# Optimization experiments

Hardware: AMD Instinct MI355X
Metric: run time of the kernel (lower is better)

Reference implementation:

```python
import jax, jax.numpy as jnp
import numpy as np
from jax import lax


def _layernorm(x, g, b, eps=1e-5):
    mu = x.mean(-1, keepdims=True)
    var = ((x - mu) ** 2).mean(-1, keepdims=True)
    return (x - mu) * lax.rsqrt(var + eps) * g + b


def _conv1d(x, w, b):
    # x: (B, T, Cin), w: (K, Cin, Cout) -> (B, T, Cout), SAME padding
    return lax.conv_general_dilated(x, w, (1,), 'SAME',
                                    dimension_numbers=('NWC', 'WIO', 'NWC')) + b


def _gated(x, wf, bf, wg, bg):
    return jax.nn.relu(_conv1d(x, wf, bf)) * jax.nn.sigmoid(_conv1d(x, wg, bg))


def setup_inputs() -> dict:
    key = jax.random.key(0)
    ks = iter(jax.random.split(key, 32))
    B, T, F, H = 32, 1024, 64, 768
    ch = H // 3
    d = {'x': jax.random.normal(next(ks), (B, T, F), jnp.float32)}
    for k in (3, 5, 7):
        d[f'conv{k}_wf'] = jax.random.normal(next(ks), (k, F, ch), jnp.float32) * 0.05
        d[f'conv{k}_bf'] = jnp.zeros((ch,), jnp.float32)
        d[f'conv{k}_wg'] = jax.random.normal(next(ks), (k, F, ch), jnp.float32) * 0.05
        d[f'conv{k}_bg'] = jnp.zeros((ch,), jnp.float32)
    d['conv_ln_g'] = jnp.ones((H,), jnp.float32)
    d['conv_ln_b'] = jnp.zeros((H,), jnp.float32)
    for name in ('gqa_wq', 'gqa_wk', 'gqa_wv', 'gqa_wp'):
        d[name] = jax.random.normal(next(ks), (2, H, H), jnp.float32) * 0.02
    d['gqa_bp'] = jnp.zeros((2, H), jnp.float32)
    d['gqa_ln_g'] = jnp.ones((2, H), jnp.float32)
    d['gqa_ln_b'] = jnp.zeros((2, H), jnp.float32)
    d['proj_w'] = jax.random.normal(next(ks), (2 * H, H), jnp.float32) * 0.02
    d['proj_b'] = jnp.zeros((H,), jnp.float32)
    d['proj_ln_g'] = jnp.ones((H,), jnp.float32)
    d['proj_ln_b'] = jnp.zeros((H,), jnp.float32)
    return d


def _gqa(h, wq, wk, wv, wp, bp, ln_g, ln_b, n_groups=4):
    B, T, H = h.shape
    G, D = n_groups, H // n_groups
    scale = D ** -0.5
    Q = (h @ wq).reshape(B, T, G, D)
    K = (h @ wk).reshape(B, T, G, D)
    V = (h @ wv).reshape(B, T, G, D)
    attn = jax.nn.softmax(jnp.einsum('bqgd,bkgd->bgqk', Q, K) * scale, axis=-1)
    out = jnp.einsum('bgqk,bkgd->bqgd', attn, V).reshape(B, T, H)
    return _layernorm(h + out @ wp + bp, ln_g, ln_b)


def reference(x, conv3_wf, conv3_bf, conv3_wg, conv3_bg,
              conv5_wf, conv5_bf, conv5_wg, conv5_bg,
              conv7_wf, conv7_bf, conv7_wg, conv7_bg,
              conv_ln_g, conv_ln_b,
              gqa_wq, gqa_wk, gqa_wv, gqa_wp, gqa_bp, gqa_ln_g, gqa_ln_b,
              proj_w, proj_b, proj_ln_g, proj_ln_b):
    # Multi-scale gated conv front end (SAME padding -> all branches length T)
    o3 = _gated(x, conv3_wf, conv3_bf, conv3_wg, conv3_bg)
    o5 = _gated(x, conv5_wf, conv5_bf, conv5_wg, conv5_bg)
    o7 = _gated(x, conv7_wf, conv7_bf, conv7_wg, conv7_bg)
    h = _layernorm(jnp.concatenate([o3, o5, o7], axis=-1), conv_ln_g, conv_ln_b)
    # Two GQA blocks
    for i in range(2):
        h = _gqa(h, gqa_wq[i], gqa_wk[i], gqa_wv[i], gqa_wp[i],
                 gqa_bp[i], gqa_ln_g[i], gqa_ln_b[i])
    # mean + population-std pooling over time
    m = h.mean(axis=1)
    s = jnp.sqrt(((h - m[:, None, :]) ** 2).mean(axis=1))
    z = jnp.concatenate([m, s], axis=-1) @ proj_w + proj_b
    return jax.nn.relu(_layernorm(z, proj_ln_g, proj_ln_b))
```

## Files before the change

kernel.cpp:

```cpp
#include <hip/hip_runtime.h>
#include <hip/hip_bf16.h>


constexpr int Bb = 32, Tt = 1024, Ff = 64, Hh = 768, Gg = 4, Dd = 192;
constexpr float EPS = 1e-5f;
constexpr int WKMAX = 448;

typedef __attribute__((ext_vector_type(8))) short short8;
typedef __attribute__((ext_vector_type(4))) float floatx4;

__device__ __forceinline__ void async_copy16(const void* g, void* l) {
  __builtin_amdgcn_global_load_lds(
      (const __attribute__((address_space(1))) unsigned int*)g,
      (__attribute__((address_space(3))) unsigned int*)l, 16, 0, 0);
}

__device__ __forceinline__ short bf16s(float f) {
  __hip_bfloat16 h = __float2bfloat16(f);
  return *(short*)&h;
}

__device__ __forceinline__ unsigned int pack_bf16(float lo, float hi) {
  return (unsigned int)(unsigned short)bf16s(lo) |
         ((unsigned int)(unsigned short)bf16s(hi) << 16);
}

__device__ __forceinline__ float2 block_reduce2(float a, float b, float* tmp) {
  int lane = threadIdx.x & 63, wid = threadIdx.x >> 6;
#pragma unroll
  for (int off = 32; off > 0; off >>= 1) {
    a += __shfl_down(a, off);
    b += __shfl_down(b, off);
  }
  if (lane == 0) { tmp[wid] = a; tmp[4 + wid] = b; }
  __syncthreads();
  if (threadIdx.x == 0) {
    tmp[0] = tmp[0] + tmp[1] + tmp[2] + tmp[3];
    tmp[4] = tmp[4] + tmp[5] + tmp[6] + tmp[7];
  }
  __syncthreads();
  float2 r; r.x = tmp[0]; r.y = tmp[4];
  return r;
}

__global__ __launch_bounds__(256) void wt_cast_kernel(
    const float* __restrict__ wq, const float* __restrict__ wk,
    const float* __restrict__ wv, const float* __restrict__ wp,
    __hip_bfloat16* __restrict__ wt) {
  const int z = blockIdx.z;
  const int m = z & 3, i = z >> 2;
  const float* src =
      (m == 0 ? wq : m == 1 ? wk : m == 2 ? wv : wp) + (size_t)i * Hh * Hh;
  const float sc = (m == 0) ? 0.0721687836f : 1.f;
  __shared__ float tile[32][33];
  const int n0 = blockIdx.x * 32, k0 = blockIdx.y * 32;
  const int tx = threadIdx.x & 31, ty = threadIdx.x >> 5;
#pragma unroll
  for (int r = 0; r < 4; r++)
    tile[ty + 8 * r][tx] = src[(size_t)(k0 + ty + 8 * r) * Hh + n0 + tx];
  __syncthreads();
#pragma unroll
  for (int r = 0; r < 4; r++)
    wt[((size_t)z * Hh + n0 + ty + 8 * r) * Hh + k0 + tx] =
        __float2bfloat16(tile[tx][ty + 8 * r] * sc);
}

__global__ __launch_bounds__(256) void wcv_cast_kernel(
    const float* __restrict__ wf3, const float* __restrict__ wg3,
    const float* __restrict__ wf5, const float* __restrict__ wg5,
    const float* __restrict__ wf7, const float* __restrict__ wg7,
    __hip_bfloat16* __restrict__ wcv) {
  int idx = blockIdx.x * 256 + threadIdx.x;
  if (idx >= 3 * 512 * WKMAX) return;
  int j = idx / (512 * WKMAX);
  int rem = idx - j * 512 * WKMAX;
  int n = rem / WKMAX, k = rem % WKMAX;
  int Kw = 3 + 2 * j;
  float v = 0.f;
  if (k < Kw * 64) {
    const float* src = (n < 256) ? (j == 0 ? wf3 : j == 1 ? wf5 : wf7)
                                 : (j == 0 ? wg3 : j == 1 ? wg5 : wg7);
    v = src[(size_t)k * 256 + (n & 255)];
  }
  wcv[idx] = __float2bfloat16(v);
}

__global__ __launch_bounds__(256) void x_cast_kernel(
    const float* __restrict__ x, short* __restrict__ x16, int n8) {
  int idx = blockIdx.x * 256 + threadIdx.x;
  if (idx >= n8) return;
  const float4 a = ((const float4*)x)[idx * 2];
  const float4 b = ((const float4*)x)[idx * 2 + 1];
  short8 o;
  o[0] = bf16s(a.x); o[1] = bf16s(a.y); o[2] = bf16s(a.z); o[3] = bf16s(a.w);
  o[4] = bf16s(b.x); o[5] = bf16s(b.y); o[6] = bf16s(b.z); o[7] = bf16s(b.w);
  ((short8*)x16)[idx] = o;
}

__global__ __launch_bounds__(256) void conv_gemm_kernel(
    const short* __restrict__ x16, const short* __restrict__ wcv,
    short* __restrict__ yraw, int b0) {
  __shared__ __align__(16) short Asl[128 * 72];
  __shared__ __align__(16) short Bsl[128 * 72];
  const int t0 = blockIdx.x * 128, n0 = blockIdx.y * 128;
  const int bl = blockIdx.z / 3, j = blockIdx.z % 3;
  const int Kw = 3 + 2 * j, pad = j + 1;
  const int bglob = b0 + bl;
  const short* wb = wcv + (size_t)j * 512 * WKMAX;
  const int tid = threadIdx.x;
  const int lane = tid & 63;
  const int w = tid >> 6, wm = w >> 1, wn = w & 1;
  const int lm = lane & 15, quad = lane >> 4;

  floatx4 acc[4][4];
#pragma unroll
  for (int i = 0; i < 4; i++)
#pragma unroll
    for (int jj = 0; jj < 4; jj++) acc[i][jj] = (floatx4)0.f;

  for (int kk = 0; kk < Kw; kk++) {
    __syncthreads();
#pragma unroll
    for (int it = 0; it < 4; it++) {
      int s = it * 256 + tid;
      int row = s >> 3, c8 = s & 7;
      int t = t0 + row + kk - pad;
      short8 av = (short8)0;
      if (t >= 0 && t < Tt)
        av = *(const short8*)&x16[((size_t)bglob * Tt + t) * Ff + c8 * 8];
      *(short8*)&Asl[row * 72 + c8 * 8] = av;
      short8 bv = *(const short8*)&wb[(size_t)(n0 + row) * WKMAX + kk * 64 +
                                      c8 * 8];
      *(short8*)&Bsl[row * 72 + c8 * 8] = bv;
    }
    __syncthreads();
#pragma unroll
    for (int ks = 0; ks < 2; ks++) {
      short8 a[4], b[4];
#pragma unroll
      for (int i = 0; i < 4; i++)
        a[i] = *(const short8*)&Asl[(wm * 64 + i * 16 + lm) * 72 + ks * 32 +
                                    quad * 8];
#pragma unroll
      for (int jj = 0; jj < 4; jj++)
        b[jj] = *(const short8*)&Bsl[(wn * 64 + jj * 16 + lm) * 72 + ks * 32 +
                                     quad * 8];
#pragma unroll
      for (int i = 0; i < 4; i++)
#pragma unroll
        for (int jj = 0; jj < 4; jj++)
          acc[i][jj] = __builtin_amdgcn_mfma_f32_16x16x32_bf16(a[i], b[jj],
                                                               acc[i][jj],
                                                               0, 0, 0);
    }
  }

  const int rbase = quad * 4;
#pragma unroll
  for (int i = 0; i < 4; i++)
#pragma unroll
    for (int jj = 0; jj < 4; jj++) {
      int mrow = t0 + wm * 64 + i * 16 + rbase;
      int ncol = n0 + wn * 64 + jj * 16 + lm;
#pragma unroll
      for (int r = 0; r < 4; r++)
        yraw[((size_t)bl * Tt + mrow + r) * 1536 + j * 512 + ncol] =
            bf16s(acc[i][jj][r]);
    }
}

__global__ __launch_bounds__(256) void gate_ln_kernel(
    const short* __restrict__ yraw, __hip_bfloat16* __restrict__ h16,
    const float* __restrict__ bf3, const float* __restrict__ bg3,
    const float* __restrict__ bf5, const float* __restrict__ bg5,
    const float* __restrict__ bf7, const float* __restrict__ bg7,
    const float* __restrict__ g, const float* __restrict__ bt) {
  __shared__ float red[8];
  const size_t row = blockIdx.x;
  float v[3], s = 0.f, ss = 0.f;
#pragma unroll
  for (int jj = 0; jj < 3; jj++) {
    int c = threadIdx.x + jj * 256;
    int br = c >> 8, cc = c & 255;
    const float* bfp = br == 0 ? bf3 : br == 1 ? bf5 : bf7;
    const float* bgp = br == 0 ? bg3 : br == 1 ? bg5 : bg7;
    __hip_bfloat16 rf = *(const __hip_bfloat16*)&yraw[row * 1536 + br * 512 + cc];
    __hip_bfloat16 rg =
        *(const __hip_bfloat16*)&yraw[row * 1536 + br * 512 + 256 + cc];
    float f = __bfloat162float(rf) + bfp[cc];
    float gt = __bfloat162float(rg) + bgp[cc];
    float a = f > 0.f ? f : 0.f;
    float t = a * (1.f / (1.f + __expf(-gt)));
    v[jj] = t; s += t; ss += t * t;
  }
  float2 r = block_reduce2(s, ss, red);
  float mu = r.x * (1.f / Hh);
  float var = r.y * (1.f / Hh) - mu * mu;
  float rs = rsqrtf(var + EPS);
#pragma unroll
  for (int jj = 0; jj < 3; jj++) {
    int c = threadIdx.x + jj * 256;
    float o = (v[jj] - mu) * rs * g[c] + bt[c];
    h16[row * Hh + c] = __float2bfloat16(o);
  }
}

__global__ __launch_bounds__(256) void res_ln_kernel(
    __hip_bfloat16* __restrict__ h16, const __hip_bfloat16* __restrict__ y,
    const float* __restrict__ bp, const float* __restrict__ g,
    const float* __restrict__ bt) {
  __shared__ float red[8];
  const size_t row = blockIdx.x;
  float v[3], s = 0.f, ss = 0.f;
#pragma unroll
  for (int jj = 0; jj < 3; jj++) {
    int c = threadIdx.x + jj * 256;
    float t = __bfloat162float(h16[row * Hh + c]) +
              __bfloat162float(y[row * Hh + c]) + bp[c];
    v[jj] = t; s += t; ss += t * t;
  }
  float2 r = block_reduce2(s, ss, red);
  float mu = r.x * (1.f / Hh);
  float var = r.y * (1.f / Hh) - mu * mu;
  float rs = rsqrtf(var + EPS);
#pragma unroll
  for (int jj = 0; jj < 3; jj++) {
    int c = threadIdx.x + jj * 256;
    float o = (v[jj] - mu) * rs * g[c] + bt[c];
    h16[row * Hh + c] = __float2bfloat16(o);
  }
}

__global__ __launch_bounds__(256) void gemm_qkv(
    const short* __restrict__ A, const short* __restrict__ Bt,
    short* __restrict__ q16, short* __restrict__ k16,
    short* __restrict__ vt16) {
  constexpr int K = 768;
  __shared__ __align__(16) short Asl[128 * 32];
  __shared__ __align__(16) short Bsl[128 * 32];
  const int n0 = blockIdx.x * 128, m0 = blockIdx.y * 128;
  const int lane = threadIdx.x & 63;
  const int w = threadIdx.x >> 6, wm = w >> 1, wn = w & 1;
  const int lm = lane & 15, quad = lane >> 4;

  floatx4 acc[4][4];
#pragma unroll
  for (int i = 0; i < 4; i++)
#pragma unroll
    for (int jj = 0; jj < 4; jj++) acc[i][jj] = (floatx4)0.f;

  for (int k0 = 0; k0 < K; k0 += 32) {
    __syncthreads();
#pragma unroll
    for (int half = 0; half < 2; half++) {
      int s = half * 256 + threadIdx.x;
      int m = s >> 2, ks = (s & 3) * 8;
      async_copy16(&A[(size_t)(m0 + m) * K + k0 + ks], &Asl[s * 8]);
      async_copy16(&Bt[(size_t)(n0 + m) * K + k0 + ks], &Bsl[s * 8]);
    }
    __syncthreads();

    short8 a[4], b[4];
#pragma unroll
    for (int i = 0; i < 4; i++)
      a[i] = *(const short8*)&Asl[(wm * 64 + i * 16 + lm) * 32 + quad * 8];
#pragma unroll
    for (int jj = 0; jj < 4; jj++)
      b[jj] = *(const short8*)&Bsl[(wn * 64 + jj * 16 + lm) * 32 + quad * 8];
#pragma unroll
    for (int i = 0; i < 4; i++)
#pragma unroll
      for (int jj = 0; jj < 4; jj++)
        acc[i][jj] = __builtin_amdgcn_mfma_f32_16x16x32_bf16(a[i], b[jj],
                                                             acc[i][jj],
                                                             0, 0, 0);
  }

  const int which = blockIdx.x / 6;
  const int rbase = quad * 4;
#pragma unroll
  for (int i = 0; i < 4; i++)
#pragma unroll
    for (int jj = 0; jj < 4; jj++) {
      int mrow = m0 + wm * 64 + i * 16 + rbase;
      int nl = n0 - which * Hh + wn * 64 + jj * 16 + lm;
      if (which == 0) {
#pragma unroll
        for (int r = 0; r < 4; r++)
          q16[(size_t)(mrow + r) * Hh + nl] = bf16s(acc[i][jj][r]);
      } else if (which == 1) {
#pragma unroll
        for (int r = 0; r < 4; r++)
          k16[(size_t)(mrow + r) * Hh + nl] = bf16s(acc[i][jj][r]);
      } else {
        int bL = mrow >> 10, t = mrow & 1023;
        int g = nl / Dd, d = nl % Dd;
        short4 sv;
        sv.x = bf16s(acc[i][jj][0]); sv.y = bf16s(acc[i][jj][1]);
        sv.z = bf16s(acc[i][jj][2]); sv.w = bf16s(acc[i][jj][3]);
        *(short4*)&vt16[(((size_t)bL * Gg + g) * Dd + d) * Tt + t] = sv;
      }
    }
}

__global__ __launch_bounds__(256) void gemm_proj(
    const short* __restrict__ A, const short* __restrict__ Bt,
    short* __restrict__ C) {
  constexpr int K = 768, N = 768;
  __shared__ __align__(16) short Asl[128 * 32];
  __shared__ __align__(16) short Bsl[128 * 32];
  const int n0 = blockIdx.x * 128, m0 = blockIdx.y * 128;
  const int lane = threadIdx.x & 63;
  const int w = threadIdx.x >> 6, wm = w >> 1, wn = w & 1;
  const int lm = lane & 15, quad = lane >> 4;

  floatx4 acc[4][4];
#pragma unroll
  for (int i = 0; i < 4; i++)
#pragma unroll
    for (int jj = 0; jj < 4; jj++) acc[i][jj] = (floatx4)0.f;

  for (int k0 = 0; k0 < K; k0 += 32) {
    __syncthreads();
#pragma unroll
    for (int half = 0; half < 2; half++) {
      int s = half * 256 + threadIdx.x;
      int m = s >> 2, ks = (s & 3) * 8;
      async_copy16(&A[(size_t)(m0 + m) * K + k0 + ks], &Asl[s * 8]);
      async_copy16(&Bt[(size_t)(n0 + m) * K + k0 + ks], &Bsl[s * 8]);
    }
    __syncthreads();

    short8 a[4], b[4];
#pragma unroll
    for (int i = 0; i < 4; i++)
      a[i] = *(const short8*)&Asl[(wm * 64 + i * 16 + lm) * 32 + quad * 8];
#pragma unroll
    for (int jj = 0; jj < 4; jj++)
      b[jj] = *(const short8*)&Bsl[(wn * 64 + jj * 16 + lm) * 32 + quad * 8];
#pragma unroll
    for (int i = 0; i < 4; i++)
#pragma unroll
      for (int jj = 0; jj < 4; jj++)
        acc[i][jj] = __builtin_amdgcn_mfma_f32_16x16x32_bf16(a[i], b[jj],
                                                             acc[i][jj],
                                                             0, 0, 0);
  }

  const int rbase = quad * 4;
#pragma unroll
  for (int i = 0; i < 4; i++)
#pragma unroll
    for (int jj = 0; jj < 4; jj++) {
      int mrow = m0 + wm * 64 + i * 16 + rbase;
      int ncol = n0 + wn * 64 + jj * 16 + lm;
#pragma unroll
      for (int r = 0; r < 4; r++)
        C[(size_t)(mrow + r) * N + ncol] = bf16s(acc[i][jj][r]);
    }
}

__global__ __launch_bounds__(256, 2) void attn_mfma(
    const short* __restrict__ q16, const short* __restrict__ k16,
    const short* __restrict__ vt16, short* __restrict__ o16, int chunk4) {
  const int bg = blockIdx.x % chunk4;
  const int qb = blockIdx.x / chunk4;
  const int b = bg >> 2, g = bg & 3;
  const int q0 = qb * 128;
  const int tid = threadIdx.x;
  const int w = tid >> 6, lane = tid & 63, lm = lane & 15, quad = lane >> 4;

  __shared__ __align__(16) short Ks[2][32 * 200];
  __shared__ __align__(16) short Vt[2][208 * 32];
  constexpr int VBUF = 208 * 32;

  for (int e = tid; e < 2 * 16 * 32; e += 256) {
    int buf = e >> 9;
    int r = e & 511;
    Vt[buf][192 * 32 + r] = (r < 32) ? (short)0x3F80 : (short)0;
  }

  short8 qf[2][6];
#pragma unroll
  for (int mt = 0; mt < 2; mt++)
#pragma unroll
    for (int ks = 0; ks < 6; ks++) {
      int tok = b * Tt + q0 + w * 32 + mt * 16 + lm;
      qf[mt][ks] = *(const short8*)&q16[(size_t)tok * Hh + g * Dd + ks * 32 +
                                        quad * 8];
    }

  floatx4 Oa[2][13];
#pragma unroll
  for (int mt = 0; mt < 2; mt++)
#pragma unroll
    for (int n = 0; n < 13; n++) Oa[mt][n] = (floatx4)0.f;

  int krow[3], kcs[3];
  const short* kgp[3];
  const short* vgp[3];
  short* vld[3];
#pragma unroll
  for (int it = 0; it < 3; it++) {
    int s = it * 256 + tid;
    krow[it] = s / 24; kcs[it] = s - krow[it] * 24;
    kgp[it] = &k16[(size_t)(b * Tt + krow[it]) * Hh + g * Dd + kcs[it] * 8];
    vgp[it] = &vt16[(((size_t)b * Gg + g) * Dd + (s >> 2)) * Tt + (s & 3) * 8];
    vld[it] = (short*)&Vt[0][0] + (size_t)s * 8;
  }

  short8 kvK[3];
#pragma unroll
  for (int it = 0; it < 3; it++) kvK[it] = *(const short8*)kgp[it];
#pragma unroll
  for (int it = 0; it < 3; it++)
    *(short8*)&Ks[0][krow[it] * 200 + kcs[it] * 8] = kvK[it];
#pragma unroll
  for (int it = 0; it < 3; it++)
    kvK[it] = *(const short8*)(kgp[it] + (size_t)32 * Hh);
#pragma unroll
  for (int it = 0; it < 3; it++) async_copy16(vgp[it], vld[it]);

  for (int i = 0; i < 32; i++) {
    const int ib = i & 1;
    __syncthreads();

    if (i + 1 < 32) {
#pragma unroll
      for (int it = 0; it < 3; it++)
        *(short8*)&Ks[ib ^ 1][krow[it] * 200 + kcs[it] * 8] = kvK[it];
      const int vo = (i + 1) * 32;
#pragma unroll
      for (int it = 0; it < 3; it++)
        async_copy16(vgp[it] + vo, vld[it] + (ib ^ 1) * VBUF);
      if (i + 2 < 32) {
        const size_t ko = (size_t)(i + 2) * 32 * Hh;
#pragma unroll
        for (int it = 0; it < 3; it++)
          kvK[it] = *(const short8*)(kgp[it] + ko);
      }
    }

    floatx4 st[2][2];
#pragma unroll
    for (int mt = 0; mt < 2; mt++)
#pragma unroll
      for (int jj = 0; jj < 2; jj++) st[mt][jj] = (floatx4)0.f;
#pragma unroll
    for (int ks = 0; ks < 6; ks++) {
      short8 k0 = *(const short8*)&Ks[ib][lm * 200 + ks * 32 + quad * 8];
      short8 k1 = *(const short8*)&Ks[ib][(16 + lm) * 200 + ks * 32 + quad * 8];
      st[0][0] = __builtin_amdgcn_mfma_f32_16x16x32_bf16(k0, qf[0][ks], st[0][0], 0, 0, 0);
      st[0][1] = __builtin_amdgcn_mfma_f32_16x16x32_bf16(k1, qf[0][ks], st[0][1], 0, 0, 0);
      st[1][0] = __builtin_amdgcn_mfma_f32_16x16x32_bf16(k0, qf[1][ks], st[1][0], 0, 0, 0);
      st[1][1] = __builtin_amdgcn_mfma_f32_16x16x32_bf16(k1, qf[1][ks], st[1][1], 0, 0, 0);
    }

    short8 ptf[2];
#pragma unroll
    for (int mt = 0; mt < 2; mt++) {
      float p[2][4];
#pragma unroll
      for (int jj = 0; jj < 2; jj++)
#pragma unroll
        for (int r = 0; r < 4; r++) p[jj][r] = __expf(st[mt][jj][r]);

      int pk00 = (int)pack_bf16(p[0][0], p[0][1]);
      int pk01 = (int)pack_bf16(p[0][2], p[0][3]);
      int pk10 = (int)pack_bf16(p[1][0], p[1][1]);
      int pk11 = (int)pack_bf16(p[1][2], p[1][3]);
      int srcA = ((quad & 1) << 5) + lm;
      int srcB = srcA + 16;
      int a0 = __shfl(pk00, srcA), a1 = __shfl(pk01, srcA);
      int a2 = __shfl(pk00, srcB), a3 = __shfl(pk01, srcB);
      int b0 = __shfl(pk10, srcA), b1 = __shfl(pk11, srcA);
      int b2 = __shfl(pk10, srcB), b3 = __shfl(pk11, srcB);
      bool hi = quad >= 2;
      union { int u[4]; short8 v; } pu;
      pu.u[0] = hi ? b0 : a0;
      pu.u[1] = hi ? b1 : a1;
      pu.u[2] = hi ? b2 : a2;
      pu.u[3] = hi ? b3 : a3;
      ptf[mt] = pu.v;
    }

#pragma unroll
    for (int n = 0; n < 13; n++) {
      short8 vf = *(const short8*)&Vt[ib][(n * 16 + lm) * 32 + quad * 8];
      Oa[0][n] = __builtin_amdgcn_mfma_f32_16x16x32_bf16(vf, ptf[0], Oa[0][n], 0, 0, 0);
      Oa[1][n] = __builtin_amdgcn_mfma_f32_16x16x32_bf16(vf, ptf[1], Oa[1][n], 0, 0, 0);
    }
  }

#pragma unroll
  for (int mt = 0; mt < 2; mt++) {
    float lval = __shfl(Oa[mt][12][0], lm);
    float inv = 1.f / lval;
    int tok = b * Tt + q0 + w * 32 + mt * 16 + lm;
#pragma unroll
    for (int n = 0; n < 12; n++) {
      short4 sv;
      sv.x = bf16s(Oa[mt][n][0] * inv);
      sv.y = bf16s(Oa[mt][n][1] * inv);
      sv.z = bf16s(Oa[mt][n][2] * inv);
      sv.w = bf16s(Oa[mt][n][3] * inv);
      *(short4*)&o16[(size_t)tok * Hh + g * Dd + n * 16 + quad * 4] = sv;
    }
  }
}

__global__ __launch_bounds__(256) void pool_stage1(
    const __hip_bfloat16* __restrict__ h16, float* __restrict__ ppart,
    int b0) {
  int idx = blockIdx.x * 256 + threadIdx.x;
  int seg = blockIdx.y;
  int bl = idx / Hh, c = idx % Hh;
  float s = 0.f, ss = 0.f;
  const __hip_bfloat16* hp = &h16[((size_t)bl * Tt + seg * 128) * Hh + c];
  for (int t = 0; t < 128; t++) {
    float v = __bfloat162float(hp[(size_t)t * Hh]);
    s += v; ss += v * v;
  }
  float* o = &ppart[(((size_t)(b0 + bl) * 8 + seg) * 2) * Hh + c];
  o[0] = s;
  o[Hh] = ss;
}

__global__ __launch_bounds__(256) void pool_stage2(
    const float* __restrict__ ppart, float* __restrict__ pool) {
  int idx = blockIdx.x * 256 + threadIdx.x;
  int b = idx / Hh, c = idx % Hh;
  float s = 0.f, ss = 0.f;
#pragma unroll
  for (int seg = 0; seg < 8; seg++) {
    const float* o = &ppart[(((size_t)b * 8 + seg) * 2) * Hh + c];
    s += o[0]; ss += o[Hh];
  }
  float mu = s * (1.f / Tt);
  float var = ss * (1.f / Tt) - mu * mu;
  pool[(size_t)b * 1536 + c] = mu;
  pool[(size_t)b * 1536 + 768 + c] = sqrtf(fmaxf(var, 0.f));
}

__global__ __launch_bounds__(256) void final_partial(
    const float* __restrict__ pool, const float* __restrict__ pw,
    float* __restrict__ part) {
  const int n = blockIdx.x * 256 + threadIdx.x;
  const int bg = blockIdx.y * 4;
  const int ks = blockIdx.z, k0 = ks * 192;
  __shared__ float ms[4][192];
  for (int e = threadIdx.x; e < 4 * 192; e += 256) {
    int bb = e / 192, kk = e % 192;
    ms[bb][kk] = pool[(size_t)(bg + bb) * 1536 + k0 + kk];
  }
  __syncthreads();
  float a0 = 0.f, a1 = 0.f, a2 = 0.f, a3 = 0.f;
  for (int kk = 0; kk < 192; kk++) {
    float wv = pw[(size_t)(k0 + kk) * Hh + n];
    a0 = fmaf(ms[0][kk], wv, a0);
    a1 = fmaf(ms[1][kk], wv, a1);
    a2 = fmaf(ms[2][kk], wv, a2);
    a3 = fmaf(ms[3][kk], wv, a3);
  }
  part[((size_t)ks * Bb + bg + 0) * Hh + n] = a0;
  part[((size_t)ks * Bb + bg + 1) * Hh + n] = a1;
  part[((size_t)ks * Bb + bg + 2) * Hh + n] = a2;
  part[((size_t)ks * Bb + bg + 3) * Hh + n] = a3;
}

__global__ __launch_bounds__(256) void final_stage2(
    const float* __restrict__ part, const float* __restrict__ pb,
    const float* __restrict__ g, const float* __restrict__ bt,
    float* __restrict__ out) {
  __shared__ float red[8];
  const int b = blockIdx.x;
  float v[3], s = 0.f, ss = 0.f;
#pragma unroll
  for (int jj = 0; jj < 3; jj++) {
    int n = threadIdx.x + jj * 256;
    float a = pb[n];
#pragma unroll
    for (int ks = 0; ks < 8; ks++) a += part[((size_t)ks * Bb + b) * Hh + n];
    v[jj] = a; s += a; ss += a * a;
  }
  float2 r = block_reduce2(s, ss, red);
  float mu = r.x * (1.f / Hh);
  float var = r.y * (1.f / Hh) - mu * mu;
  float rs = rsqrtf(var + EPS);
#pragma unroll
  for (int jj = 0; jj < 3; jj++) {
    int n = threadIdx.x + jj * 256;
    float o = (v[jj] - mu) * rs * g[n] + bt[n];
    out[(size_t)b * Hh + n] = o > 0.f ? o : 0.f;
  }
}

extern "C" void kernel_launch(void* const* d_in, const int* in_sizes, int n_in,
                              void* d_out, int out_size, void* d_ws,
                              size_t ws_size, hipStream_t stream) {
  (void)in_sizes; (void)n_in; (void)out_size;
  const float* x = (const float*)d_in[0];
  const float* cw[3][4];
  for (int j = 0; j < 3; j++)
    for (int p2 = 0; p2 < 4; p2++) cw[j][p2] = (const float*)d_in[1 + j * 4 + p2];
  const float* conv_ln_g = (const float*)d_in[13];
  const float* conv_ln_b = (const float*)d_in[14];
  const float* wq = (const float*)d_in[15];
  const float* wk = (const float*)d_in[16];
  const float* wv = (const float*)d_in[17];
  const float* wp = (const float*)d_in[18];
  const float* bp = (const float*)d_in[19];
  const float* lng = (const float*)d_in[20];
  const float* lnb = (const float*)d_in[21];
  const float* proj_w = (const float*)d_in[22];
  const float* proj_b = (const float*)d_in[23];
  const float* proj_ln_g = (const float*)d_in[24];
  const float* proj_ln_b = (const float*)d_in[25];
  float* out = (float*)d_out;

  const size_t perb = (size_t)Tt * Hh;
  const size_t fixedB = 8ull * Hh * Hh * 2 + 3ull * 512 * WKMAX * 2 +
                        (size_t)Bb * Tt * Ff * 2 + (size_t)Bb * 2 * Hh * 4 +
                        (size_t)Bb * 8 * 2 * Hh * 4 + 8ull * Bb * Hh * 4;
  int chunk = Bb;
  while (chunk > 1 && 8ull * perb * chunk + fixedB > ws_size) chunk >>= 1;

  const size_t crow = perb * (size_t)chunk;
  char* p = (char*)d_ws;
  __hip_bfloat16* h16 = (__hip_bfloat16*)p;  p += crow * 2;
  short* q16 = (short*)p;            p += crow * 2;
  short* k16 = (short*)p;            p += crow * 2;
  short* v16t = (short*)p;           p += crow * 2;
  short* yraw16 = q16;
  short* y16 = k16;
  __hip_bfloat16* wt = (__hip_bfloat16*)p;   p += 8ull * Hh * Hh * 2;
  __hip_bfloat16* wcv = (__hip_bfloat16*)p;  p += 3ull * 512 * WKMAX * 2;
  short* x16 = (short*)p;            p += (size_t)Bb * Tt * Ff * 2;
  float* pool = (float*)p;           p += (size_t)Bb * 2 * Hh * 4;
  float* ppart = (float*)p;          p += (size_t)Bb * 8 * 2 * Hh * 4;
  float* fpart = (float*)p;

  wt_cast_kernel<<<dim3(24, 24, 8), 256, 0, stream>>>(wq, wk, wv, wp, wt);
  wcv_cast_kernel<<<(3 * 512 * WKMAX + 255) / 256, 256, 0, stream>>>(
      cw[0][0], cw[0][2], cw[1][0], cw[1][2], cw[2][0], cw[2][2], wcv);
  x_cast_kernel<<<(Bb * Tt * Ff / 8 + 255) / 256, 256, 0, stream>>>(
      x, x16, Bb * Tt * Ff / 8);

  const short* wts = (const short*)wt;

  for (int b0 = 0; b0 < Bb; b0 += chunk) {
    const int M = chunk * Tt;

    conv_gemm_kernel<<<dim3(Tt / 128, 4, chunk * 3), 256, 0, stream>>>(
        x16, (const short*)wcv, yraw16, b0);
    gate_ln_kernel<<<M, 256, 0, stream>>>(
        yraw16, h16, cw[0][1], cw[0][3], cw[1][1], cw[1][3], cw[2][1],
        cw[2][3], conv_ln_g, conv_ln_b);

    for (int i = 0; i < 2; i++) {
      const short* wqkv = wts + (size_t)(i * 4) * Hh * Hh;
      const short* wtp = wts + (size_t)(i * 4 + 3) * Hh * Hh;
      gemm_qkv<<<dim3(18, M / 128), 256, 0, stream>>>((const short*)h16, wqkv,
                                                      q16, k16, v16t);
      attn_mfma<<<dim3(chunk * Gg * (Tt / 128)), 256, 0, stream>>>(
          q16, k16, v16t, q16, chunk * Gg);
      gemm_proj<<<dim3(6, M / 128), 256, 0, stream>>>(q16, wtp, y16);
      res_ln_kernel<<<M, 256, 0, stream>>>(h16, (const __hip_bfloat16*)y16,
                                           bp + (size_t)i * Hh,
                                           lng + (size_t)i * Hh,
                                           lnb + (size_t)i * Hh);
    }

    pool_stage1<<<dim3((chunk * Hh) / 256, 8), 256, 0, stream>>>(h16, ppart,
                                                                 b0);
  }

  pool_stage2<<<(Bb * Hh) / 256, 256, 0, stream>>>(ppart, pool);
  final_partial<<<dim3(3, 8, 8), 256, 0, stream>>>(pool, proj_w, fpart);
  final_stage2<<<Bb, 256, 0, stream>>>(fpart, proj_b, proj_ln_g, proj_ln_b,
                                       out);
}
```

Measured before the change: 990.6 us.

## Replace QKV and proj GEMMs with 256x256 tile, 4-stage async pipelined kernel

Merges the QKV and output-projection GEMMs into one templated kernel. It uses 256x256 tiles with 8 waves and a 4-deep ring of LDS buffers filled by async global-to-LDS copies, synchronised with explicit vmcnt waits and barriers. It also adds an XCD-aware block-index swizzle, a swizzled LDS layout to avoid bank conflicts, and raised wave priority around the MFMA block. The aim is to hide global load latency and raise MFMA utilisation, at the cost of 128KB of LDS and high register pressure that may limit occupancy.

```diff
diff --git a/kernel.cpp b/kernel.cpp
--- a/kernel.cpp
+++ b/kernel.cpp
@@ -231,133 +231,144 @@
   }
 }
 
-__global__ __launch_bounds__(256) void gemm_qkv(
+template <int MODE>
+__global__ __launch_bounds__(512, 2) void gemm_8ph(
     const short* __restrict__ A, const short* __restrict__ Bt,
-    short* __restrict__ q16, short* __restrict__ k16,
-    short* __restrict__ vt16) {
+    short* __restrict__ out_q, short* __restrict__ out_k,
+    short* __restrict__ out_v) {
   constexpr int K = 768;
-  __shared__ __align__(16) short Asl[128 * 32];
-  __shared__ __align__(16) short Bsl[128 * 32];
-  const int n0 = blockIdx.x * 128, m0 = blockIdx.y * 128;
-  const int lane = threadIdx.x & 63;
-  const int w = threadIdx.x >> 6, wm = w >> 1, wn = w & 1;
+  constexpr int NT = K / 32;
+  constexpr int NB = (MODE == 0) ? 9 : 3;
+  __shared__ __align__(16) short lds[4][16384];
+
+  const int nwg = gridDim.x;
+  const int qq = nwg >> 3, rr = nwg & 7;
+  const int xcd = blockIdx.x & 7, bidx = blockIdx.x >> 3;
+  const int swz =
+      (xcd < rr ? xcd * (qq + 1) : rr * (qq + 1) + (xcd - rr) * qq) + bidx;
+  const int nb = swz % NB, mb = swz / NB;
+  const int n0 = nb * 256, m0 = mb * 256;
+
+  const int tid = threadIdx.x;
+  const int lane = tid & 63, w = tid >> 6;
   const int lm = lane & 15, quad = lane >> 4;
-
-  floatx4 acc[4][4];
-#pragma unroll
-  for (int i = 0; i < 4; i++)
-#pragma unroll
-    for (int jj = 0; jj < 4; jj++) acc[i][jj] = (floatx4)0.f;
-
-  for (int k0 = 0; k0 < K; k0 += 32) {
-    __syncthreads();
-#pragma unroll
-    for (int half = 0; half < 2; half++) {
-      int s = half * 256 + threadIdx.x;
-      int m = s >> 2, ks = (s & 3) * 8;
-      async_copy16(&A[(size_t)(m0 + m) * K + k0 + ks], &Asl[s * 8]);
-      async_copy16(&Bt[(size_t)(n0 + m) * K + k0 + ks], &Bsl[s * 8]);
-    }
-    __syncthreads();
-
-    short8 a[4], b[4];
-#pragma unroll
-    for (int i = 0; i < 4; i++)
-      a[i] = *(const short8*)&Asl[(wm * 64 + i * 16 + lm) * 32 + quad * 8];
-#pragma unroll
-    for (int jj = 0; jj < 4; jj++)
-      b[jj] = *(const short8*)&Bsl[(wn * 64 + jj * 16 + lm) * 32 + quad * 8];
-#pragma unroll
-    for (int i = 0; i < 4; i++)
-#pragma unroll
-      for (int jj = 0; jj < 4; jj++)
-        acc[i][jj] = __builtin_amdgcn_mfma_f32_16x16x32_bf16(a[i], b[jj],
-                                                             acc[i][jj],
-                                                             0, 0, 0);
-  }
-
-  const int which = blockIdx.x / 6;
+  const int wm = w >> 2, wn = w & 3;
+
+  const short* sA[2];
+  const short* sB[2];
+  int dst[2];
+#pragma unroll
+  for (int li = 0; li < 2; li++) {
+    int l = li * 512 + tid;
+    int reg = l >> 6, cs = l & 63;
+    int cs2 = cs ^ (((cs >> 5) & 1) << 1);
+    int row = (reg << 4) + (cs2 >> 2);
+    int col = (cs2 & 3) << 3;
+    sA[li] = A + (size_t)(m0 + row) * K + col;
+    sB[li] = Bt + (size_t)(n0 + row) * K + col;
+    dst[li] = l * 8;
+  }
+
+#define STAGE8(kt, ring)                                   \
+  {                                                        \
+    const int _o = (kt) * 32;                              \
+    async_copy16(sA[0] + _o, &lds[ring][dst[0]]);          \
+    async_copy16(sB[0] + _o, &lds[ring][8192 + dst[0]]);   \
+    async_copy16(sA[1] + _o, &lds[ring][dst[1]]);          \
+    async_copy16(sB[1] + _o, &lds[ring][8192 + dst[1]]);   \
+  }
+
+  const int lane_sh = (lm * 32 + quad * 8) ^ ((lm >> 3) << 4);
+
+  floatx4 acc[8][4];
+#pragma unroll
+  for (int i = 0; i < 8; i++)
+#pragma unroll
+    for (int j = 0; j < 4; j++) acc[i][j] = (floatx4)0.f;
+
+  STAGE8(0, 0);
+  STAGE8(1, 1);
+  STAGE8(2, 2);
+  asm volatile("s_waitcnt vmcnt(8)" ::: "memory");
+  asm volatile("s_barrier" ::: "memory");
+  __builtin_amdgcn_sched_barrier(0);
+
+  for (int t = 0; t < NT; t++) {
+    const int ring = t & 3;
+    if (t + 3 < NT) STAGE8(t + 3, (t + 3) & 3);
+
+    short8 a[8], b[4];
+#pragma unroll
+    for (int i = 0; i < 8; i++)
+      a[i] = *(const short8*)&lds[ring][(wm * 8 + i) * 512 + lane_sh];
+#pragma unroll
+    for (int j = 0; j < 4; j++)
+      b[j] = *(const short8*)&lds[ring][8192 + (wn * 4 + j) * 512 + lane_sh];
+
+    __builtin_amdgcn_s_setprio(1);
+#pragma unroll
+    for (int i = 0; i < 8; i++)
+#pragma unroll
+      for (int j = 0; j < 4; j++)
+        acc[i][j] = __builtin_amdgcn_mfma_f32_16x16x32_bf16(a[i], b[j],
+                                                            acc[i][j],
+                                                            0, 0, 0);
+    __builtin_amdgcn_s_setprio(0);
+
+    if (t < NT - 1) {
+      if (t < NT - 3)
+        asm volatile("s_waitcnt vmcnt(8)" ::: "memory");
+      else if (t == NT - 3)
+        asm volatile("s_waitcnt vmcnt(4)" ::: "memory");
+      else
+        asm volatile("s_waitcnt vmcnt(0)" ::: "memory");
+      asm volatile("s_barrier" ::: "memory");
+      __builtin_amdgcn_sched_barrier(0);
+    }
+  }
+#undef STAGE8
+
   const int rbase = quad * 4;
-#pragma unroll
-  for (int i = 0; i < 4; i++)
-#pragma unroll
-    for (int jj = 0; jj < 4; jj++) {
-      int mrow = m0 + wm * 64 + i * 16 + rbase;
-      int nl = n0 - which * Hh + wn * 64 + jj * 16 + lm;
-      if (which == 0) {
+  if (MODE == 1) {
+#pragma unroll
+    for (int i = 0; i < 8; i++) {
+      const int mrow = m0 + wm * 128 + i * 16 + rbase;
+#pragma unroll
+      for (int j = 0; j < 4; j++) {
+        const int ncol = n0 + wn * 64 + j * 16 + lm;
 #pragma unroll
         for (int r = 0; r < 4; r++)
-          q16[(size_t)(mrow + r) * Hh + nl] = bf16s(acc[i][jj][r]);
-      } else if (which == 1) {
-#pragma unroll
-        for (int r = 0; r < 4; r++)
-          k16[(size_t)(mrow + r) * Hh + nl] = bf16s(acc[i][jj][r]);
-      } else {
-        int bL = mrow >> 10, t = mrow & 1023;
-        int g = nl / Dd, d = nl % Dd;
-        short4 sv;
-        sv.x = bf16s(acc[i][jj][0]); sv.y = bf16s(acc[i][jj][1]);
-        sv.z = bf16s(acc[i][jj][2]); sv.w = bf16s(acc[i][jj][3]);
-        *(short4*)&vt16[(((size_t)bL * Gg + g) * Dd + d) * Tt + t] = sv;
+          out_q[(size_t)(mrow + r) * Hh + ncol] = bf16s(acc[i][j][r]);
       }
     }
-}
-
-__global__ __launch_bounds__(256) void gemm_proj(
-    const short* __restrict__ A, const short* __restrict__ Bt,
-    short* __restrict__ C) {
-  constexpr int K = 768, N = 768;
-  __shared__ __align__(16) short Asl[128 * 32];
-  __shared__ __align__(16) short Bsl[128 * 32];
-  const int n0 = blockIdx.x * 128, m0 = blockIdx.y * 128;
-  const int lane = threadIdx.x & 63;
-  const int w = threadIdx.x >> 6, wm = w >> 1, wn = w & 1;
-  const int lm = lane & 15, quad = lane >> 4;
-
-  floatx4 acc[4][4];
-#pragma unroll
-  for (int i = 0; i < 4; i++)
-#pragma unroll
-    for (int jj = 0; jj < 4; jj++) acc[i][jj] = (floatx4)0.f;
-
-  for (int k0 = 0; k0 < K; k0 += 32) {
-    __syncthreads();
-#pragma unroll
-    for (int half = 0; half < 2; half++) {
-      int s = half * 256 + threadIdx.x;
-      int m = s >> 2, ks = (s & 3) * 8;
-      async_copy16(&A[(size_t)(m0 + m) * K + k0 + ks], &Asl[s * 8]);
-      async_copy16(&Bt[(size_t)(n0 + m) * K + k0 + ks], &Bsl[s * 8]);
-    }
-    __syncthreads();
-
-    short8 a[4], b[4];
-#pragma unroll
-    for (int i = 0; i < 4; i++)
-      a[i] = *(const short8*)&Asl[(wm * 64 + i * 16 + lm) * 32 + quad * 8];
-#pragma unroll
-    for (int jj = 0; jj < 4; jj++)
-      b[jj] = *(const short8*)&Bsl[(wn * 64 + jj * 16 + lm) * 32 + quad * 8];
-#pragma unroll
-    for (int i = 0; i < 4; i++)
-#pragma unroll
-      for (int jj = 0; jj < 4; jj++)
-        acc[i][jj] = __builtin_amdgcn_mfma_f32_16x16x32_bf16(a[i], b[jj],
-                                                             acc[i][jj],
-                                                             0, 0, 0);
-  }
-
-  const int rbase = quad * 4;
-#pragma unroll
-  for (int i = 0; i < 4; i++)
-#pragma unroll
-    for (int jj = 0; jj < 4; jj++) {
-      int mrow = m0 + wm * 64 + i * 16 + rbase;
-      int ncol = n0 + wn * 64 + jj * 16 + lm;
-#pragma unroll
-      for (int r = 0; r < 4; r++)
-        C[(size_t)(mrow + r) * N + ncol] = bf16s(acc[i][jj][r]);
-    }
+  } else {
+    const int which = nb / 3;
+    const int nbase = (nb % 3) * 256;
+#pragma unroll
+    for (int i = 0; i < 8; i++) {
+      const int mrow = m0 + wm * 128 + i * 16 + rbase;
+#pragma unroll
+      for (int j = 0; j < 4; j++) {
+        const int nl = nbase + wn * 64 + j * 16 + lm;
+        if (which == 0) {
+#pragma unroll
+          for (int r = 0; r < 4; r++)
+            out_q[(size_t)(mrow + r) * Hh + nl] = bf16s(acc[i][j][r]);
+        } else if (which == 1) {
+#pragma unroll
+          for (int r = 0; r < 4; r++)
+            out_k[(size_t)(mrow + r) * Hh + nl] = bf16s(acc[i][j][r]);
+        } else {
+          const int bL = mrow >> 10, ttok = mrow & 1023;
+          const int g = nl / Dd, d = nl % Dd;
+          short4 sv;
+          sv.x = bf16s(acc[i][j][0]); sv.y = bf16s(acc[i][j][1]);
+          sv.z = bf16s(acc[i][j][2]); sv.w = bf16s(acc[i][j][3]);
+          *(short4*)&out_v[(((size_t)bL * Gg + g) * Dd + d) * Tt + ttok] = sv;
+        }
+      }
+    }
+  }
 }
 
 __global__ __launch_bounds__(256, 2) void attn_mfma(
@@ -660,11 +671,12 @@
     for (int i = 0; i < 2; i++) {
       const short* wqkv = wts + (size_t)(i * 4) * Hh * Hh;
       const short* wtp = wts + (size_t)(i * 4 + 3) * Hh * Hh;
-      gemm_qkv<<<dim3(18, M / 128), 256, 0, stream>>>((const short*)h16, wqkv,
-                                                      q16, k16, v16t);
+      gemm_8ph<0><<<dim3(9 * (M / 256)), 512, 0, stream>>>(
+          (const short*)h16, wqkv, q16, k16, v16t);
       attn_mfma<<<dim3(chunk * Gg * (Tt / 128)), 256, 0, stream>>>(
           q16, k16, v16t, q16, chunk * Gg);
-      gemm_proj<<<dim3(6, M / 128), 256, 0, stream>>>(q16, wtp, y16);
+      gemm_8ph<1><<<dim3(3 * (M / 256)), 512, 0, stream>>>(
+          q16, wtp, y16, nullptr, nullptr);
       res_ln_kernel<<<M, 256, 0, stream>>>(h16, (const __hip_bfloat16*)y16,
                                            bp + (size_t)i * Hh,
                                            lng + (size_t)i * Hh,
```

After: 934.2 us. 1.06x faster.
